# Kernel tuning notes

Hardware: AMD Instinct MI355X
Metric: run time of the kernel (lower is better)

## Reference

```python
import jax, jax.numpy as jnp
import numpy as np

D_ENC = 512
D_DEC = 512
JOINT = 512
VOCAB = 1024


def setup_inputs() -> dict:
    key = jax.random.key(0)
    ks = jax.random.split(key, 7)
    B, T, U = 4, 256, 64
    s_enc = 1.0 / np.sqrt(D_ENC)
    s_dec = 1.0 / np.sqrt(D_DEC)
    s_out = 1.0 / np.sqrt(JOINT)
    return {
        "encoder_out": jax.random.normal(ks[0], (B, T, 1, D_ENC), dtype=jnp.float32),
        "decoder_out": jax.random.normal(ks[1], (B, 1, U, D_DEC), dtype=jnp.float32),
        # torch.nn.Linear stores weight as (out, in); uniform(-1/sqrt(in), 1/sqrt(in))
        "W_enc": jax.random.uniform(ks[2], (JOINT, D_ENC), jnp.float32, -s_enc, s_enc),
        "b_enc": jax.random.uniform(ks[3], (JOINT,), jnp.float32, -s_enc, s_enc),
        "W_dec": jax.random.uniform(ks[4], (JOINT, D_DEC), jnp.float32, -s_dec, s_dec),
        "W_out": jax.random.uniform(ks[5], (VOCAB, JOINT), jnp.float32, -s_out, s_out),
        "b_out": jax.random.uniform(ks[6], (VOCAB,), jnp.float32, -s_out, s_out),
    }


def reference(encoder_out, decoder_out, W_enc, b_enc, W_dec, W_out, b_out):
    # Project each side in its small shape first (B,T,1,J) and (B,1,U,J),
    # then broadcast-add over (T,U), tanh, output GEMM -> (B,T,U,V).
    enc = jnp.einsum("btud,jd->btuj", encoder_out, W_enc) + b_enc  # (B,T,1,J)
    dec = jnp.einsum("btud,jd->btuj", decoder_out, W_dec)          # (B,1,U,J)
    h = jnp.tanh(enc + dec)                                        # (B,T,U,J)
    return jnp.einsum("btuj,vj->btuv", h, W_out) + b_out           # (B,T,U,V)
```

## Files before the change

kernel.cpp:

```cpp
#include <hip/hip_runtime.h>
#include <hip/hip_bf16.h>


typedef __attribute__((ext_vector_type(8))) short short8;
typedef __attribute__((ext_vector_type(4))) float f32x4;
typedef __attribute__((ext_vector_type(16))) float f32x16;

#define SZ0 524288
#define SZ1 131072
#define SZ2 262144
#define SZ3 512
#define SZ4 262144
#define SZ5 524288
#define SZ6 1024
#define CU0 0
#define CU1 524288
#define CU2 655360
#define CU3 917504
#define CU4 918016
#define CU5 1180160
#define CU6 1704448
#define CTOT 1705472

__global__ void detect_kernel(const void* p0, const void* p1, const void* p2,
                              const void* p3, const void* p4, const void* p5,
                              const void* p6, int* flags) {
  const void* ps[7] = {p0, p1, p2, p3, p4, p5, p6};
  const int sz[7] = {SZ0, SZ1, SZ2, SZ3, SZ4, SZ5, SZ6};
  const int w = threadIdx.x >> 6;
  const int l = threadIdx.x & 63;
  if (w >= 7) return;
  const unsigned short* u = (const unsigned short*)ps[w];
  const int lim = sz[w] < 1024 ? sz[w] : 1024;
  int bad = 0;
  for (int j = l; j < lim; j += 64) {
    const unsigned e = (u[j] >> 7) & 0xFFu;
    if (e >= 0x8Eu) bad = 1;
  }
  const unsigned long long b = __ballot(bad);
  if (l == 0) flags[w] = (b != 0ULL) ? 1 : 0;
}

__global__ __launch_bounds__(256) void convert_kernel(
    const void* p0, const void* p1, const void* p2, const void* p3,
    const void* p4, const void* p5, const void* p6,
    const int* __restrict__ flags, __hip_bfloat16* __restrict__ dst) {
  const int gid = blockIdx.x * 256 + threadIdx.x;
  if (gid >= CTOT) return;
  int t, local;
  const void* p;
  if (gid < CU1)      { t = 0; local = gid - CU0; p = p0; }
  else if (gid < CU2) { t = 1; local = gid - CU1; p = p1; }
  else if (gid < CU3) { t = 2; local = gid - CU2; p = p2; }
  else if (gid < CU4) { t = 3; local = gid - CU3; p = p3; }
  else if (gid < CU5) { t = 4; local = gid - CU4; p = p4; }
  else if (gid < CU6) { t = 5; local = gid - CU5; p = p5; }
  else                { t = 6; local = gid - CU6; p = p6; }
  __hip_bfloat16 v;
  if (flags[t])
    v = __float2bfloat16(((const float*)p)[local]);
  else
    v = ((const __hip_bfloat16*)p)[local];
  dst[gid] = v;
}

__device__ __forceinline__ void gemm_bt_body(
    const __hip_bfloat16* __restrict__ A, const __hip_bfloat16* __restrict__ Bw,
    const __hip_bfloat16* __restrict__ bias, float* __restrict__ C,
    int M, int N, int K, int bid,
    __hip_bfloat16* sA, __hip_bfloat16* sB) {
  const int tid = threadIdx.x;
  const int w = tid >> 6;
  const int l = tid & 63;
  const int ntiles = N >> 7;
  const int mt = bid / ntiles;
  const int nt = bid % ntiles;
  const int m0 = mt << 7;
  const int n0 = nt << 7;
  const int wm = (w >> 1) << 6;
  const int wn = (w & 1) << 6;
  const int r16 = l & 15;
  const int q = l >> 4;

  f32x4 acc[4][4] = {};

  const int srow_in = l >> 3;
  const int scol = (l & 7) << 3;

  for (int k0 = 0; k0 < K; k0 += 64) {
#pragma unroll
    for (int i = 0; i < 4; ++i) {
      const int c = (w << 2) + i;
      const int row = (c << 3) + srow_in;
      const __hip_bfloat16* gA = A + (size_t)(m0 + row) * K + k0 + scol;
      const __hip_bfloat16* gB = Bw + (size_t)(n0 + row) * K + k0 + scol;
      __builtin_amdgcn_global_load_lds(
          (const __attribute__((address_space(1))) void*)gA,
          (__attribute__((address_space(3))) void*)(sA + (c << 9) + (l << 3)),
          16, 0, 0);
      __builtin_amdgcn_global_load_lds(
          (const __attribute__((address_space(1))) void*)gB,
          (__attribute__((address_space(3))) void*)(sB + (c << 9) + (l << 3)),
          16, 0, 0);
    }
    __syncthreads();

#pragma unroll
    for (int kk = 0; kk < 2; ++kk) {
      const int kc = (kk << 5) + (q << 3);
      short8 af[4], bf[4];
#pragma unroll
      for (int mi = 0; mi < 4; ++mi)
        af[mi] = *(const short8*)(sA + (wm + (mi << 4) + r16) * 64 + kc);
#pragma unroll
      for (int ni = 0; ni < 4; ++ni)
        bf[ni] = *(const short8*)(sB + (wn + (ni << 4) + r16) * 64 + kc);
#pragma unroll
      for (int mi = 0; mi < 4; ++mi)
#pragma unroll
        for (int ni = 0; ni < 4; ++ni)
          acc[mi][ni] = __builtin_amdgcn_mfma_f32_16x16x32_bf16(
              af[mi], bf[ni], acc[mi][ni], 0, 0, 0);
    }
    __syncthreads();
  }

#pragma unroll
  for (int ni = 0; ni < 4; ++ni) {
    const int col = n0 + wn + (ni << 4) + r16;
    const float bc = bias ? __bfloat162float(bias[col]) : 0.0f;
#pragma unroll
    for (int mi = 0; mi < 4; ++mi) {
      const int rowb = m0 + wm + (mi << 4) + (q << 2);
#pragma unroll
      for (int i = 0; i < 4; ++i)
        C[(size_t)(rowb + i) * N + col] = acc[mi][ni][i] + bc;
    }
  }
}

__global__ __launch_bounds__(256) void proj_kernel(
    const __hip_bfloat16* __restrict__ enc, const __hip_bfloat16* __restrict__ Wenc,
    const __hip_bfloat16* __restrict__ benc,
    const __hip_bfloat16* __restrict__ dec, const __hip_bfloat16* __restrict__ Wdec,
    const __hip_bfloat16* __restrict__ Wout, __hip_bfloat16* __restrict__ WT,
    float* __restrict__ Pe, float* __restrict__ Pd) {
  __shared__ __align__(16) __hip_bfloat16 sA[128 * 64];
  __shared__ __align__(16) __hip_bfloat16 sB[128 * 64];
  if (blockIdx.x < 32) {
    gemm_bt_body(enc, Wenc, benc, Pe, 1024, 512, 512, blockIdx.x, sA, sB);
  } else if (blockIdx.x < 40) {
    gemm_bt_body(dec, Wdec, nullptr, Pd, 256, 512, 512, blockIdx.x - 32, sA, sB);
  } else {
    const int bid = blockIdx.x - 40;
#pragma unroll
    for (int i = 0; i < 32; ++i) {
      const int cid = (bid << 13) + (i << 8) + threadIdx.x;
      const int n = cid >> 6;
      const int c = cid & 63;
      *(short8*)(WT + (((size_t)c << 10) + n) * 8) =
          *(const short8*)(Wout + (size_t)n * 512 + (c << 3));
    }
  }
}

__global__ __launch_bounds__(512, 2) void gemm_joint(
    const float* __restrict__ Pe, const float* __restrict__ Pd,
    const __hip_bfloat16* __restrict__ WT,
    const __hip_bfloat16* __restrict__ bias, float* __restrict__ out) {
  __shared__ __align__(16) __hip_bfloat16 sA[2][2048 * 8];
  __shared__ __align__(16) __hip_bfloat16 sB[2][2048 * 8];

  const int t = threadIdx.x;
  const int w = t >> 6;
  const int l = t & 63;
  const int l31 = l & 31;
  const int q2 = l >> 5;
  const int mb = blockIdx.x >> 2;
  const int nb = blockIdx.x & 3;
  const int m0 = mb << 8;
  const int n0 = nb << 8;
  const int wm = (w >> 2) << 7;
  const int wn = (w & 3) << 6;

  const int arow = t & 255;
  const int acb = (t >> 8) << 2;
  const int e = (mb << 2) + (arow >> 6);
  const int dd = ((mb >> 6) << 6) | (arow & 63);

  f32x4 rPe[4][2], rPd[4][2];
  auto issueA = [&](int kt) {
    const float* peR = Pe + (size_t)e * 512 + (kt << 6);
    const float* pdR = Pd + (size_t)dd * 512 + (kt << 6);
#pragma unroll
    for (int j = 0; j < 4; ++j) {
      const int off = (acb + j) << 3;
      rPe[j][0] = *(const f32x4*)(peR + off);
      rPe[j][1] = *(const f32x4*)(peR + off + 4);
      rPd[j][0] = *(const f32x4*)(pdR + off);
      rPd[j][1] = *(const f32x4*)(pdR + off + 4);
    }
  };

  auto writeA = [&](int b) {
#pragma unroll
    for (int j = 0; j < 4; ++j) {
      short8 hv;
#pragma unroll
      for (int x = 0; x < 4; ++x) {
        float sv = rPe[j][0][x] + rPd[j][0][x];
        float u = __expf(2.0f * sv);
        float tv = 1.0f - 2.0f * __builtin_amdgcn_rcpf(u + 1.0f);
        __hip_bfloat16 hb = __float2bfloat16(tv);
        hv[x] = *(const short*)&hb;
        sv = rPe[j][1][x] + rPd[j][1][x];
        u = __expf(2.0f * sv);
        tv = 1.0f - 2.0f * __builtin_amdgcn_rcpf(u + 1.0f);
        hb = __float2bfloat16(tv);
        hv[4 + x] = *(const short*)&hb;
      }
      *(short8*)(&sA[b][0] + ((((acb + j) << 8) + arow) << 3)) = hv;
    }
  };

  auto issueB = [&](int kt, int b, int h) {
    const int slot = (h << 9) + t;
    const int c = slot >> 8;
    const int n = slot & 255;
    const __hip_bfloat16* src =
        WT + (((size_t)((kt << 3) + c) << 10) + n0 + n) * 8;
    __builtin_amdgcn_global_load_lds(
        (const __attribute__((address_space(1))) void*)src,
        (__attribute__((address_space(3))) void*)(&sB[b][0] + (slot << 3)),
        16, 0, 0);
  };

  issueA(0);
#pragma unroll
  for (int h = 0; h < 4; ++h) issueB(0, 0, h);
  asm volatile("s_waitcnt vmcnt(4)" ::: "memory");
  __builtin_amdgcn_sched_barrier(0);
  writeA(0);
  asm volatile("s_waitcnt lgkmcnt(0) vmcnt(0)" ::: "memory");
  __builtin_amdgcn_sched_barrier(0);
  __builtin_amdgcn_s_barrier();
  __builtin_amdgcn_sched_barrier(0);

  f32x16 acc[4][2] = {};

#define READS(s)                                                             \
  {                                                                          \
    const int c = ((s) << 1) + q2;                                           \
    _Pragma("unroll") for (int mi = 0; mi < 4; ++mi) af[mi] =                \
        *(const short8*)(&sA[b][0] +                                         \
                         (((c << 8) + wm + (mi << 5) + l31) << 3));          \
    _Pragma("unroll") for (int ni = 0; ni < 2; ++ni) bf[ni] =                \
        *(const short8*)(&sB[b][0] +                                         \
                         (((c << 8) + wn + (ni << 5) + l31) << 3));          \
  }
#define MFMA8                                                                \
  _Pragma("unroll") for (int mi = 0; mi < 4; ++mi)                           \
      _Pragma("unroll") for (int ni = 0; ni < 2; ++ni) acc[mi][ni] =         \
          __builtin_amdgcn_mfma_f32_32x32x16_bf16(af[mi], bf[ni],            \
                                                  acc[mi][ni], 0, 0, 0);
#define PHASE_SYNC_PRE                                                       \
  __builtin_amdgcn_s_barrier();                                              \
  asm volatile("s_waitcnt lgkmcnt(0)" ::: "memory");                         \
  __builtin_amdgcn_sched_barrier(0);                                         \
  __builtin_amdgcn_s_setprio(1);
#define PHASE_SYNC_POST                                                      \
  __builtin_amdgcn_s_setprio(0);                                             \
  __builtin_amdgcn_sched_barrier(0);                                         \
  __builtin_amdgcn_s_barrier();                                              \
  __builtin_amdgcn_sched_barrier(0);

#pragma unroll
  for (int kt = 0; kt < 8; ++kt) {
    const int b = kt & 1;
    short8 af[4], bf[2];

    if (kt < 7) issueA(kt + 1);
    READS(0)
    PHASE_SYNC_PRE
    MFMA8
    PHASE_SYNC_POST

    if (kt < 7) { issueB(kt + 1, b ^ 1, 0); issueB(kt + 1, b ^ 1, 1); }
    READS(1)
    PHASE_SYNC_PRE
    MFMA8
    PHASE_SYNC_POST

    if (kt < 7) { issueB(kt + 1, b ^ 1, 2); issueB(kt + 1, b ^ 1, 3); }
    READS(2)
    PHASE_SYNC_PRE
    MFMA8
    PHASE_SYNC_POST

    READS(3)
    if (kt < 7) {
      asm volatile("s_waitcnt vmcnt(4)" ::: "memory");
      __builtin_amdgcn_sched_barrier(0);
      writeA(b ^ 1);
    }
    __builtin_amdgcn_s_barrier();
    asm volatile("s_waitcnt lgkmcnt(0)" ::: "memory");
    __builtin_amdgcn_sched_barrier(0);
    __builtin_amdgcn_s_setprio(1);
    MFMA8
    __builtin_amdgcn_s_setprio(0);
    asm volatile("s_waitcnt vmcnt(0)" ::: "memory");
    __builtin_amdgcn_sched_barrier(0);
    __builtin_amdgcn_s_barrier();
    __builtin_amdgcn_sched_barrier(0);
  }
#undef READS
#undef MFMA8
#undef PHASE_SYNC_PRE
#undef PHASE_SYNC_POST

#pragma unroll
  for (int ni = 0; ni < 2; ++ni) {
    const int col = n0 + wn + (ni << 5) + l31;
    const float bc = __bfloat162float(bias[col]);
#pragma unroll
    for (int mi = 0; mi < 4; ++mi) {
#pragma unroll
      for (int rr = 0; rr < 16; ++rr) {
        const int row = m0 + wm + (mi << 5) + (rr & 3) + ((rr >> 2) << 3) +
                        (q2 << 2);
        out[(size_t)row * 1024 + col] = acc[mi][ni][rr] + bc;
      }
    }
  }
}

extern "C" void kernel_launch(void* const* d_in, const int* in_sizes, int n_in,
                              void* d_out, int out_size, void* d_ws,
                              size_t ws_size, hipStream_t stream) {
  char* ws = (char*)d_ws;
  int* flags = (int*)ws;
  __hip_bfloat16* cp = (__hip_bfloat16*)(ws + 256);
  float* Pe = (float*)(ws + (4ull << 20));
  float* Pd = (float*)(ws + (6ull << 20));
  __hip_bfloat16* WT = (__hip_bfloat16*)(ws + (8ull << 20));

  detect_kernel<<<dim3(1), dim3(512), 0, stream>>>(
      d_in[0], d_in[1], d_in[2], d_in[3], d_in[4], d_in[5], d_in[6], flags);
  convert_kernel<<<dim3((CTOT + 255) / 256), dim3(256), 0, stream>>>(
      d_in[0], d_in[1], d_in[2], d_in[3], d_in[4], d_in[5], d_in[6], flags, cp);

  const __hip_bfloat16* enc_c = cp + CU0;
  const __hip_bfloat16* dec_c = cp + CU1;
  const __hip_bfloat16* Wenc_c = cp + CU2;
  const __hip_bfloat16* benc_c = cp + CU3;
  const __hip_bfloat16* Wdec_c = cp + CU4;
  const __hip_bfloat16* Wout_c = cp + CU5;
  const __hip_bfloat16* bout_c = cp + CU6;

  proj_kernel<<<dim3(48), dim3(256), 0, stream>>>(
      enc_c, Wenc_c, benc_c, dec_c, Wdec_c, Wout_c, WT, Pe, Pd);
  gemm_joint<<<dim3(1024), dim3(512), 0, stream>>>(
      Pe, Pd, WT, bout_c, (float*)d_out);
}
```

Before: 436.0 us.

## Read transposed decoder projection in joint GEMM and rebalance prefetch phases

The decoder-projection GEMM now also writes a transposed copy (PdT) to the workspace. The joint kernel reads that copy with per-element loads that are contiguous across adjacent threads, replacing per-thread 32-byte row reads at a 2 KB stride. The A-operand prefetch is split into two halves spread over the first two MFMA phases, and all four B loads-to-LDS are moved into the third phase. The trade-off is many more scalar load instructions per thread and an extra strided transposed store in the projection kernel.

```diff
diff --git a/kernel.cpp b/kernel.cpp
--- a/kernel.cpp
+++ b/kernel.cpp
@@ -67,7 +67,7 @@
 __device__ __forceinline__ void gemm_bt_body(
     const __hip_bfloat16* __restrict__ A, const __hip_bfloat16* __restrict__ Bw,
     const __hip_bfloat16* __restrict__ bias, float* __restrict__ C,
-    int M, int N, int K, int bid,
+    float* __restrict__ CT, int M, int N, int K, int bid,
     __hip_bfloat16* sA, __hip_bfloat16* sB) {
   const int tid = threadIdx.x;
   const int w = tid >> 6;
@@ -133,8 +133,11 @@
     for (int mi = 0; mi < 4; ++mi) {
       const int rowb = m0 + wm + (mi << 4) + (q << 2);
 #pragma unroll
-      for (int i = 0; i < 4; ++i)
-        C[(size_t)(rowb + i) * N + col] = acc[mi][ni][i] + bc;
+      for (int i = 0; i < 4; ++i) {
+        const float v = acc[mi][ni][i] + bc;
+        C[(size_t)(rowb + i) * N + col] = v;
+        if (CT) CT[(size_t)col * M + rowb + i] = v;
+      }
     }
   }
 }
@@ -144,13 +147,15 @@
     const __hip_bfloat16* __restrict__ benc,
     const __hip_bfloat16* __restrict__ dec, const __hip_bfloat16* __restrict__ Wdec,
     const __hip_bfloat16* __restrict__ Wout, __hip_bfloat16* __restrict__ WT,
-    float* __restrict__ Pe, float* __restrict__ Pd) {
+    float* __restrict__ Pe, float* __restrict__ Pd, float* __restrict__ PdT) {
   __shared__ __align__(16) __hip_bfloat16 sA[128 * 64];
   __shared__ __align__(16) __hip_bfloat16 sB[128 * 64];
   if (blockIdx.x < 32) {
-    gemm_bt_body(enc, Wenc, benc, Pe, 1024, 512, 512, blockIdx.x, sA, sB);
+    gemm_bt_body(enc, Wenc, benc, Pe, nullptr, 1024, 512, 512, blockIdx.x,
+                 sA, sB);
   } else if (blockIdx.x < 40) {
-    gemm_bt_body(dec, Wdec, nullptr, Pd, 256, 512, 512, blockIdx.x - 32, sA, sB);
+    gemm_bt_body(dec, Wdec, nullptr, Pd, PdT, 256, 512, 512, blockIdx.x - 32,
+                 sA, sB);
   } else {
     const int bid = blockIdx.x - 40;
 #pragma unroll
@@ -165,7 +170,7 @@
 }
 
 __global__ __launch_bounds__(512, 2) void gemm_joint(
-    const float* __restrict__ Pe, const float* __restrict__ Pd,
+    const float* __restrict__ Pe, const float* __restrict__ PdT,
     const __hip_bfloat16* __restrict__ WT,
     const __hip_bfloat16* __restrict__ bias, float* __restrict__ out) {
   __shared__ __align__(16) __hip_bfloat16 sA[2][2048 * 8];
@@ -187,18 +192,21 @@
   const int acb = (t >> 8) << 2;
   const int e = (mb << 2) + (arow >> 6);
   const int dd = ((mb >> 6) << 6) | (arow & 63);
-
-  f32x4 rPe[4][2], rPd[4][2];
-  auto issueA = [&](int kt) {
+  const float* pdTb = PdT + dd;
+
+  f32x4 rPe[4][2];
+  float rPd[4][8];
+  auto issueA = [&](int kt, int half) {
     const float* peR = Pe + (size_t)e * 512 + (kt << 6);
-    const float* pdR = Pd + (size_t)dd * 512 + (kt << 6);
-#pragma unroll
-    for (int j = 0; j < 4; ++j) {
+#pragma unroll
+    for (int jj = 0; jj < 2; ++jj) {
+      const int j = (half << 1) + jj;
       const int off = (acb + j) << 3;
       rPe[j][0] = *(const f32x4*)(peR + off);
       rPe[j][1] = *(const f32x4*)(peR + off + 4);
-      rPd[j][0] = *(const f32x4*)(pdR + off);
-      rPd[j][1] = *(const f32x4*)(pdR + off + 4);
+#pragma unroll
+      for (int x = 0; x < 8; ++x)
+        rPd[j][x] = pdTb[(size_t)((kt << 6) + off + x) << 8];
     }
   };
 
@@ -208,12 +216,12 @@
       short8 hv;
 #pragma unroll
       for (int x = 0; x < 4; ++x) {
-        float sv = rPe[j][0][x] + rPd[j][0][x];
+        float sv = rPe[j][0][x] + rPd[j][x];
         float u = __expf(2.0f * sv);
         float tv = 1.0f - 2.0f * __builtin_amdgcn_rcpf(u + 1.0f);
         __hip_bfloat16 hb = __float2bfloat16(tv);
         hv[x] = *(const short*)&hb;
-        sv = rPe[j][1][x] + rPd[j][1][x];
+        sv = rPe[j][1][x] + rPd[j][x + 4];
         u = __expf(2.0f * sv);
         tv = 1.0f - 2.0f * __builtin_amdgcn_rcpf(u + 1.0f);
         hb = __float2bfloat16(tv);
@@ -235,7 +243,8 @@
         16, 0, 0);
   };
 
-  issueA(0);
+  issueA(0, 0);
+  issueA(0, 1);
 #pragma unroll
   for (int h = 0; h < 4; ++h) issueB(0, 0, h);
   asm volatile("s_waitcnt vmcnt(4)" ::: "memory");
@@ -279,19 +288,22 @@
     const int b = kt & 1;
     short8 af[4], bf[2];
 
-    if (kt < 7) issueA(kt + 1);
+    if (kt < 7) issueA(kt + 1, 0);
     READS(0)
     PHASE_SYNC_PRE
     MFMA8
     PHASE_SYNC_POST
 
-    if (kt < 7) { issueB(kt + 1, b ^ 1, 0); issueB(kt + 1, b ^ 1, 1); }
+    if (kt < 7) issueA(kt + 1, 1);
     READS(1)
     PHASE_SYNC_PRE
     MFMA8
     PHASE_SYNC_POST
 
-    if (kt < 7) { issueB(kt + 1, b ^ 1, 2); issueB(kt + 1, b ^ 1, 3); }
+    if (kt < 7) {
+      issueB(kt + 1, b ^ 1, 0); issueB(kt + 1, b ^ 1, 1);
+      issueB(kt + 1, b ^ 1, 2); issueB(kt + 1, b ^ 1, 3);
+    }
     READS(2)
     PHASE_SYNC_PRE
     MFMA8
@@ -344,6 +356,7 @@
   float* Pe = (float*)(ws + (4ull << 20));
   float* Pd = (float*)(ws + (6ull << 20));
   __hip_bfloat16* WT = (__hip_bfloat16*)(ws + (8ull << 20));
+  float* PdT = (float*)(ws + (9ull << 20));
 
   detect_kernel<<<dim3(1), dim3(512), 0, stream>>>(
       d_in[0], d_in[1], d_in[2], d_in[3], d_in[4], d_in[5], d_in[6], flags);
@@ -359,7 +372,7 @@
   const __hip_bfloat16* bout_c = cp + CU6;
 
   proj_kernel<<<dim3(48), dim3(256), 0, stream>>>(
-      enc_c, Wenc_c, benc_c, dec_c, Wdec_c, Wout_c, WT, Pe, Pd);
+      enc_c, Wenc_c, benc_c, dec_c, Wdec_c, Wout_c, WT, Pe, Pd, PdT);
   gemm_joint<<<dim3(1024), dim3(512), 0, stream>>>(
-      Pe, Pd, WT, bout_c, (float*)d_out);
-}
+      Pe, PdT, WT, bout_c, (float*)d_out);
+}
```

Result: faster. 406.6 us (-6.7%).
